# Kernel tuning notes

Measured on AMD Instinct MI355X. Metric: run time of the kernel, lower is better.

The kernel has to match this reference:

```python
import jax, jax.numpy as jnp
import numpy as np

K = 8                      # batch_k
NONZERO_CUTOFF = 1.4       # nonzero_loss_cutoff
MARGIN = 1.0               # F.triplet_margin_loss default (module's margin arg is unused)
PD_EPS = 1e-6              # torch pairwise_distance eps


def setup_inputs() -> dict:
    key = jax.random.key(0)
    x = jax.random.normal(key, (4096, 128), dtype=jnp.float32)
    return {"x": x}


def _sample_indices(x, key):
    """Distance-weighted negative sampling; returns (a_idx, p_idx, n_idx), each [n*(K-1)]."""
    n, d = x.shape
    # per-row L2 normalize (eps added to norm, as in original)
    xn = x / (jnp.sqrt(jnp.sum(x * x, axis=1, keepdims=True)) + 1e-5)
    # pairwise euclidean distance; identity added under sqrt exactly as original
    sq = jnp.sum(xn * xn, axis=1, keepdims=True)               # [n,1]
    dist2 = sq + sq.T - 2.0 * (xn @ xn.T)                       # [n,n]
    dist = jnp.sqrt(dist2 + jnp.eye(n, dtype=x.dtype))          # [n,n]
    # distance-weighted sampling log-weights (Wu et al.)
    log_w = (2.0 - d) * jnp.log(dist) - (d - 3) / 2.0 * jnp.log(1.0 - 0.25 * dist * dist)
    w = jnp.exp(log_w - jnp.max(log_w))
    # block mask: same-block pairs excluded
    block = jnp.arange(n) // K                                  # [n]
    mask = (block[:, None] != block[None, :]).astype(x.dtype)
    w = w * mask * (dist < NONZERO_CUTOFF).astype(x.dtype)
    row_sum = jnp.sum(w, axis=1, keepdims=True)
    # rows where weights are degenerate fall back to uniform (original's try/except)
    valid = jnp.isfinite(row_sum) & (row_sum > 0) & jnp.all(jnp.isfinite(w), axis=1, keepdims=True)
    logits = jnp.where(valid, jnp.where(w > 0, jnp.log(w), -jnp.inf), 0.0)   # [n,n]
    # batched categorical sampling via Gumbel-max: K-1 negatives per anchor
    g = jax.random.gumbel(key, (n, K - 1, n), dtype=jnp.float32)
    n_idx = jnp.argmax(logits[:, None, :] + g, axis=-1).reshape(-1)          # [n*(K-1)]
    # anchor/positive pairs: for each i, all other members of its block
    r = jnp.arange(n) % K                                       # position in block
    off = jnp.arange(K - 1)
    p_off = jnp.where(off[None, :] < r[:, None], off[None, :], off[None, :] + 1)
    p_idx = (block[:, None] * K + p_off).reshape(-1)            # [n*(K-1)]
    a_idx = jnp.repeat(jnp.arange(n), K - 1)                    # [n*(K-1)]
    return a_idx, p_idx, n_idx


def reference(x) -> jnp.ndarray:
    key = jax.random.key(42)
    a_idx, p_idx, n_idx = _sample_indices(x, key)
    a, p, ng = x[a_idx], x[p_idx], x[n_idx]
    d_ap = jnp.sqrt(jnp.sum((a - p + PD_EPS) ** 2, axis=1))
    d_an = jnp.sqrt(jnp.sum((a - ng + PD_EPS) ** 2, axis=1))
    return jnp.mean(jnp.maximum(d_ap - d_an + MARGIN, 0.0))
```

## Files before the change

### kernel.cpp

```cpp
#include <hip/hip_runtime.h>
#include <stdint.h>

#define NROWS 4096
#define DIM   128
#define KB    8
#define NS    7
#define TCH   16
#define NSEG  4
#define NPAIR 2048
#define HALF_CNT 58720256u

typedef __bf16 v8bf __attribute__((ext_vector_type(8)));
typedef float  v4f  __attribute__((ext_vector_type(4)));

__device__ __forceinline__ uint32_t rotl32(uint32_t x, int r) {
    return (x << r) | (x >> (32 - r));
}

__device__ __forceinline__ void threefry2x32(uint32_t c0, uint32_t c1,
                                             uint32_t& o0, uint32_t& o1) {
    const uint32_t ks0 = 0u;
    const uint32_t ks1 = 42u;
    const uint32_t ks2 = 0x1BD11BDAu ^ ks0 ^ ks1;
    uint32_t x0 = c0 + ks0;
    uint32_t x1 = c1 + ks1;
#define TF_R(r) { x0 += x1; x1 = rotl32(x1, r); x1 ^= x0; }
    TF_R(13) TF_R(15) TF_R(26) TF_R(6)
    x0 += ks1; x1 += ks2 + 1u;
    TF_R(17) TF_R(29) TF_R(16) TF_R(24)
    x0 += ks2; x1 += ks0 + 2u;
    TF_R(13) TF_R(15) TF_R(26) TF_R(6)
    x0 += ks0; x1 += ks1 + 3u;
    TF_R(17) TF_R(29) TF_R(16) TF_R(24)
    x0 += ks1; x1 += ks2 + 4u;
    TF_R(13) TF_R(15) TF_R(26) TF_R(6)
    x0 += ks2; x1 += ks0 + 5u;
#undef TF_R
    o0 = x0; o1 = x1;
}

__device__ __forceinline__ float gumbel_of(uint32_t b) {
    float f = __uint_as_float((b >> 9) | 0x3f800000u) - 1.0f;
    float u = f + 1.17549435e-38f;
    float l1 = __log2f(u);
    float inner = -0.69314718055994531f * l1;
    float l2 = __log2f(inner);
    return -0.69314718055994531f * l2;
}

__global__ void knorm(const float* __restrict__ x, __bf16* __restrict__ xb,
                      float* __restrict__ sqv) {
    const int i = blockIdx.x;
    const int t = threadIdx.x;
    float2 v = ((const float2*)(x + (size_t)i * DIM))[t];
    float s = v.x * v.x + v.y * v.y;
#pragma unroll
    for (int m = 32; m > 0; m >>= 1) s += __shfl_xor(s, m, 64);
    float norm = sqrtf(s) + 1e-5f;
    float ox = v.x / norm, oy = v.y / norm;
    union { __bf16 b[2]; uint32_t u; } ph;
    ph.b[0] = (__bf16)ox; ph.b[1] = (__bf16)oy;
    ((uint32_t*)xb)[i * 64 + t] = ph.u;
    float s2 = ox * ox + oy * oy;
#pragma unroll
    for (int m = 32; m > 0; m >>= 1) s2 += __shfl_xor(s2, m, 64);
    if (t == 0) sqv[i] = s2;
}

__global__ __launch_bounds__(256, 4) void kdist(
        const __bf16* __restrict__ xb, const float* __restrict__ sqv,
        int* __restrict__ cnt, unsigned short* __restrict__ t16,
        float2* __restrict__ nwp) {
    const int lane  = threadIdx.x & 63;
    const int chunk = (blockIdx.x << 2) + (threadIdx.x >> 6);
    const int grp   = blockIdx.y;
    const int rlo = lane & 15;
    const int khi = lane >> 4;
    const unsigned int below = (1u << rlo) - 1u;

    const int afr = grp * 8 + (rlo >> 1) + ((rlo & 1) << 11);
    v8bf ah[4];
#pragma unroll
    for (int ks = 0; ks < 4; ++ks)
        ah[ks] = *(const v8bf*)(xb + (size_t)afr * DIM + ks * 32 + khi * 8);

    const int base = grp * 8 + khi * 2;
    float sqA[4];
    sqA[0] = sqv[base];
    sqA[1] = sqv[base + 2048];
    sqA[2] = sqv[base + 1];
    sqA[3] = sqv[base + 2049];

    const int rbA = ((base)     * 16 + chunk) << 8;
    const int rbB = ((base + 1) * 16 + chunk) << 8;
    unsigned int cA = 0, cB = 0;

    const int tcol0 = chunk * 256 + rlo;

    v8bf bhn[4];
    float sqn;
    {
        const size_t boff = (size_t)tcol0 * DIM + khi * 8;
#pragma unroll
        for (int ks = 0; ks < 4; ++ks) bhn[ks] = *(const v8bf*)(xb + boff + ks * 32);
        sqn = sqv[tcol0];
    }

#pragma unroll 1
    for (int cg = 0; cg < 16; ++cg) {
        v8bf bhc[4];
#pragma unroll
        for (int ks = 0; ks < 4; ++ks) bhc[ks] = bhn[ks];
        const float sqB = sqn;
        const int tcol = tcol0 + cg * 16;

        if (cg < 15) {
            const size_t boff = (size_t)(tcol + 16) * DIM + khi * 8;
#pragma unroll
            for (int ks = 0; ks < 4; ++ks) bhn[ks] = *(const v8bf*)(xb + boff + ks * 32);
            sqn = sqv[tcol + 16];
        }

        v4f acc = {0.f, 0.f, 0.f, 0.f};
#pragma unroll
        for (int ks = 0; ks < 4; ++ks)
            acc = __builtin_amdgcn_mfma_f32_16x16x32_bf16(ah[ks], bhc[ks], acc, 0, 0, 0);

        const int tBlk = tcol >> 3;
        const bool bd0 = (tBlk != grp);
        const bool bd1 = (tBlk != grp + 256);

        float nw[4];
        bool  ic[4];
#pragma unroll
        for (int q = 0; q < 4; ++q) {
            float d2  = fmaf(-2.0f, acc[q], sqA[q] + sqB);
            float l1  = __log2f(d2);
            float t2  = fmaf(-0.25f, d2, 1.0f);
            float l2  = __log2f(t2);
            float wiv = exp2f(fmaf(63.0f, l1, 62.5f * l2));
            bool incl = (d2 < 1.96f) && ((q & 1) ? bd1 : bd0);
            ic[q] = incl;
            nw[q] = incl ? -wiv : -INFINITY;
        }

        const bool uA = ic[0] | ic[1];
        const bool uB = ic[2] | ic[3];
        unsigned long long ballA = __ballot(uA);
        unsigned long long ballB = __ballot(uB);
        unsigned int subA = (unsigned int)((ballA >> (khi * 16)) & 0xFFFFull);
        unsigned int subB = (unsigned int)((ballB >> (khi * 16)) & 0xFFFFull);
        if (uA) {
            int slot = rbA + (int)cA + __popc(subA & below);
            t16[slot] = (unsigned short)tcol;
            nwp[slot] = make_float2(nw[0], nw[1]);
        }
        if (uB) {
            int slot = rbB + (int)cB + __popc(subB & below);
            t16[slot] = (unsigned short)tcol;
            nwp[slot] = make_float2(nw[2], nw[3]);
        }
        cA += (unsigned int)__popc(subA);
        cB += (unsigned int)__popc(subB);
    }

    if (rlo == 0) {
        cnt[base * 16 + chunk]       = (int)cA;
        cnt[(base + 1) * 16 + chunk] = (int)cB;
    }
}

__global__ __launch_bounds__(256, 8) void kgum(
        const int* __restrict__ cnt, const unsigned short* __restrict__ t16,
        const float2* __restrict__ nwp,
        float* __restrict__ pV, int* __restrict__ pI) {
    const int wid  = threadIdx.x >> 6;
    const int rid  = (blockIdx.x << 2) + wid;
    const int p    = rid >> 4;
    const int lane = threadIdx.x & 63;
    const int j    = lane & 7;
    const int eo   = lane >> 3;
    const bool jv  = (j < 7);
    const uint32_t pb = ((uint32_t)p * 7u + (uint32_t)j) << 12;

    __shared__ unsigned short st[4][256];
    __shared__ float2         snw[4][256];

    const int n  = cnt[rid];
    const int rb = rid << 8;

    for (int s = lane; s < n; s += 64) {
        st[wid][s]  = t16[rb + s];
        snw[wid][s] = nwp[rb + s];
    }
    __syncthreads();

    float bkA = INFINITY, bkB = INFINITY;
    int   btA = 0x7FFFFFFF, btB = 0x7FFFFFFF;

#pragma unroll 1
    for (int e = eo; e < n; e += 8) {
        const uint32_t t = st[wid][e];
        const float2 nw  = snw[wid][e];
        const uint32_t L = pb + t;
        uint32_t o0, o1;
        threefry2x32(L, L + HALF_CNT, o0, o1);
        float fA = __uint_as_float((o0 >> 9) | 0x3f800000u) - 1.0f;
        float fB = __uint_as_float((o1 >> 9) | 0x3f800000u) - 1.0f;
        float l1A = __log2f(fA + 1.17549435e-38f);
        float l1B = __log2f(fB + 1.17549435e-38f);
        float kA = jv ? l1A * nw.x : INFINITY;
        float kB = jv ? l1B * nw.y : INFINITY;
        const int ti = (int)t;
        if (kA < bkA || (kA == bkA && ti < btA)) { bkA = kA; btA = ti; }
        if (kB < bkB || (kB == bkB && ti < btB)) { bkB = kB; btB = ti; }
    }

#pragma unroll
    for (int m = 8; m < 64; m <<= 1) {
        float v2 = __shfl_xor(bkA, m, 64);
        int   t2 = __shfl_xor(btA, m, 64);
        if (v2 < bkA || (v2 == bkA && t2 < btA)) { bkA = v2; btA = t2; }
        v2 = __shfl_xor(bkB, m, 64);
        t2 = __shfl_xor(btB, m, 64);
        if (v2 < bkB || (v2 == bkB && t2 < btB)) { bkB = v2; btB = t2; }
    }

    __shared__ float sV[4][2][NS];
    __shared__ int   sT[4][2][NS];
    if (lane < NS) {
        sV[wid][0][lane] = bkA; sT[wid][0][lane] = btA;
        sV[wid][1][lane] = bkB; sT[wid][1][lane] = btB;
    }
    __syncthreads();
    if (threadIdx.x < 2 * NS) {
        const int r = threadIdx.x / NS, jj = threadIdx.x - r * NS;
        float v = sV[0][r][jj];
        int   t = sT[0][r][jj];
#pragma unroll
        for (int w = 1; w < 4; ++w) {
            float v2 = sV[w][r][jj];
            int   t2 = sT[w][r][jj];
            if (v2 < v || (v2 == v && t2 < t)) { v = v2; t = t2; }
        }
        const int cgrp = blockIdx.x & 3;
        size_t s = ((size_t)(p + r * 2048) * NS + jj) * NSEG + cgrp;
        pV[s] = v; pI[s] = t;
    }
}

__global__ void kcombine(const float* __restrict__ pV, const int* __restrict__ pI,
                         int* __restrict__ nidx, int nc) {
    int s = blockIdx.x * 256 + threadIdx.x;
    if (s >= NROWS * NS) return;
    float bv = INFINITY;
    int bi = 0x7FFFFFFF;
    for (int c = 0; c < nc; ++c) {
        float v = pV[(size_t)s * nc + c];
        int idx = pI[(size_t)s * nc + c];
        if (v < bv || (v == bv && idx < bi)) { bv = v; bi = idx; }
    }
    nidx[s] = (bv == INFINITY) ? -1 : bi;
}

__global__ __launch_bounds__(256, 2) void ksample(
        const __bf16* __restrict__ xb, const float* __restrict__ sqv,
        float* __restrict__ pV, int* __restrict__ pI) {
    const int lane  = threadIdx.x & 63;
    const int chunk = (blockIdx.x << 2) + (threadIdx.x >> 6);
    const int grp   = blockIdx.y;
    const int rlo = lane & 15;
    const int khi = lane >> 4;

    const int afr = grp * 8 + (rlo >> 1) + ((rlo & 1) << 11);
    v8bf ah[4];
#pragma unroll
    for (int ks = 0; ks < 4; ++ks)
        ah[ks] = *(const v8bf*)(xb + (size_t)afr * DIM + ks * 32 + khi * 8);
    const int base = grp * 8 + khi * 2;
    float sqA[4];
    sqA[0] = sqv[base];
    sqA[1] = sqv[base + 2048];
    sqA[2] = sqv[base + 1];
    sqA[3] = sqv[base + 2049];
    const uint32_t P0 = (uint32_t)base;
    const uint32_t P1 = (uint32_t)(base + 1);

    float    bestV[4][NS];
    uint32_t bestP[4];
#pragma unroll
    for (int q = 0; q < 4; ++q) {
        bestP[q] = 0u;
#pragma unroll
        for (int j = 0; j < NS; ++j) bestV[q][j] = INFINITY;
    }
    const int tcol0 = chunk * 256 + rlo;

    v8bf bhn[4];
    float sqn;
    {
        const size_t boff = (size_t)tcol0 * DIM + khi * 8;
#pragma unroll
        for (int ks = 0; ks < 4; ++ks) bhn[ks] = *(const v8bf*)(xb + boff + ks * 32);
        sqn = sqv[tcol0];
    }

#pragma unroll 1
    for (int cg = 0; cg < 16; ++cg) {
        v8bf bhc[4];
#pragma unroll
        for (int ks = 0; ks < 4; ++ks) bhc[ks] = bhn[ks];
        const float sqB = sqn;
        const int tcol = tcol0 + cg * 16;
        if (cg < 15) {
            const size_t boff = (size_t)(tcol + 16) * DIM + khi * 8;
#pragma unroll
            for (int ks = 0; ks < 4; ++ks) bhn[ks] = *(const v8bf*)(xb + boff + ks * 32);
            sqn = sqv[tcol + 16];
        }
        v4f acc = {0.f, 0.f, 0.f, 0.f};
#pragma unroll
        for (int ks = 0; ks < 4; ++ks)
            acc = __builtin_amdgcn_mfma_f32_16x16x32_bf16(ah[ks], bhc[ks], acc, 0, 0, 0);
        const int tBlk = tcol >> 3;
        const bool bd0 = (tBlk != grp);
        const bool bd1 = (tBlk != grp + 256);
        float nw[4];
#pragma unroll
        for (int q = 0; q < 4; ++q) {
            float d2  = fmaf(-2.0f, acc[q], sqA[q] + sqB);
            float l1  = __log2f(d2);
            float t2  = fmaf(-0.25f, d2, 1.0f);
            float l2  = __log2f(t2);
            float wiv = exp2f(fmaf(63.0f, l1, 62.5f * l2));
            bool incl = (d2 < 1.96f) && ((q & 1) ? bd1 : bd0);
            nw[q] = incl ? -wiv : -INFINITY;
        }
        const uint32_t tB = (uint32_t)tcol;
#pragma unroll
        for (int j = 0; j < NS; ++j) {
            uint32_t L0 = ((P0 * 7u + (uint32_t)j) << 12) + tB;
            uint32_t L1 = ((P1 * 7u + (uint32_t)j) << 12) + tB;
            uint32_t o0, o1, o2, o3;
            threefry2x32(L0, L0 + HALF_CNT, o0, o1);
            threefry2x32(L1, L1 + HALF_CNT, o2, o3);
            float vv[4];
            vv[0] = __log2f(__uint_as_float((o0 >> 9) | 0x3f800000u) - 1.0f + 1.17549435e-38f) * nw[0];
            vv[1] = __log2f(__uint_as_float((o1 >> 9) | 0x3f800000u) - 1.0f + 1.17549435e-38f) * nw[1];
            vv[2] = __log2f(__uint_as_float((o2 >> 9) | 0x3f800000u) - 1.0f + 1.17549435e-38f) * nw[2];
            vv[3] = __log2f(__uint_as_float((o3 >> 9) | 0x3f800000u) - 1.0f + 1.17549435e-38f) * nw[3];
            const uint32_t keep = ~(0xFu << (4 * j));
            const uint32_t put  = ((uint32_t)cg) << (4 * j);
#pragma unroll
            for (int q = 0; q < 4; ++q) {
                bool lt = vv[q] < bestV[q][j];
                uint32_t np = (bestP[q] & keep) | put;
                bestV[q][j] = lt ? vv[q] : bestV[q][j];
                bestP[q]    = lt ? np : bestP[q];
            }
        }
    }
#pragma unroll
    for (int q = 0; q < 4; ++q) {
        const int a = base + (q >> 1) + ((q & 1) << 11);
#pragma unroll
        for (int j = 0; j < NS; ++j) {
            float v = bestV[q][j];
            int idx = tcol0 + (int)((bestP[q] >> (4 * j)) & 0xFu) * 16;
#pragma unroll
            for (int m = 1; m < 16; m <<= 1) {
                float v2 = __shfl_xor(v, m, 16);
                int   i2 = __shfl_xor(idx, m, 16);
                if (v2 < v || (v2 == v && i2 < idx)) { v = v2; idx = i2; }
            }
            if (rlo == 0) {
                size_t s = ((size_t)a * NS + j) * TCH + chunk;
                pV[s] = v;
                pI[s] = idx;
            }
        }
    }
}

__global__ void kfixup(int* __restrict__ nidx) {
    const int i = blockIdx.x;
    if (nidx[(size_t)i * NS] >= 0) return;
    const int lane = threadIdx.x;
    for (int j = 0; j < NS; ++j) {
        float bv = -INFINITY;
        int bi = 0x7FFFFFFF;
        for (int t = lane; t < NROWS; t += 64) {
            uint32_t o0, o1;
            float g;
            if (i < 2048) {
                uint32_t L = (((uint32_t)(i * NS + j)) << 12) + (uint32_t)t;
                threefry2x32(L, L + HALF_CNT, o0, o1);
                g = gumbel_of(o0);
            } else {
                uint32_t L = (((uint32_t)((i - 2048) * NS + j)) << 12) + (uint32_t)t;
                threefry2x32(L, L + HALF_CNT, o0, o1);
                g = gumbel_of(o1);
            }
            if (g > bv) { bv = g; bi = t; }
        }
#pragma unroll
        for (int m = 1; m < 64; m <<= 1) {
            float v2 = __shfl_xor(bv, m, 64);
            int   i2 = __shfl_xor(bi, m, 64);
            if (v2 > bv || (v2 == bv && i2 < bi)) { bv = v2; bi = i2; }
        }
        if (lane == 0) nidx[i * NS + j] = bi;
    }
}

__global__ void kloss(const float* __restrict__ x, const int* __restrict__ nidx,
                      float* __restrict__ loss) {
    int s = blockIdx.x * 256 + threadIdx.x;
    if (s >= NROWS * NS) return;
    int i = s / NS, j = s - i * NS;
    int r = i & (KB - 1), blk = i >> 3;
    int po = (j < r) ? j : j + 1;
    int p = blk * KB + po;
    int n = nidx[s] & (NROWS - 1);
    const float4* A  = (const float4*)(x + (size_t)i * DIM);
    const float4* P  = (const float4*)(x + (size_t)p * DIM);
    const float4* Ng = (const float4*)(x + (size_t)n * DIM);
    float sap = 0.0f, san = 0.0f;
#pragma unroll 8
    for (int k = 0; k < DIM / 4; ++k) {
        float4 a = A[k], pv = P[k], nv = Ng[k];
        float d;
        d = a.x - pv.x + 1e-6f; sap += d * d;
        d = a.y - pv.y + 1e-6f; sap += d * d;
        d = a.z - pv.z + 1e-6f; sap += d * d;
        d = a.w - pv.w + 1e-6f; sap += d * d;
        d = a.x - nv.x + 1e-6f; san += d * d;
        d = a.y - nv.y + 1e-6f; san += d * d;
        d = a.z - nv.z + 1e-6f; san += d * d;
        d = a.w - nv.w + 1e-6f; san += d * d;
    }
    loss[s] = fmaxf(sqrtf(sap) - sqrtf(san) + 1.0f, 0.0f);
}

__global__ void kreduce(const float* __restrict__ loss, float* __restrict__ out) {
    __shared__ float part[4];
    const int tid = threadIdx.x;
    float sum = 0.0f;
    for (int s = tid; s < NROWS * NS; s += 256) sum += loss[s];
#pragma unroll
    for (int m = 32; m > 0; m >>= 1) sum += __shfl_xor(sum, m, 64);
    if ((tid & 63) == 0) part[tid >> 6] = sum;
    __syncthreads();
    if (tid == 0) out[0] = (part[0] + part[1] + part[2] + part[3]) / 28672.0f;
}

extern "C" void kernel_launch(void* const* d_in, const int* in_sizes, int n_in,
                              void* d_out, int out_size, void* d_ws, size_t ws_size,
                              hipStream_t stream) {
    const float* x = (const float*)d_in[0];
    float* out = (float*)d_out;

    uint8_t* w = (uint8_t*)d_ws;
    size_t off = 0;
    auto take = [&](size_t bytes) {
        void* p = w + off;
        off = (off + bytes + 255) & ~(size_t)255;
        return p;
    };
    __bf16* xb   = (__bf16*)take((size_t)NROWS * DIM * 2);
    float*  sqv  = (float*)take((size_t)NROWS * 4);
    int*    nidx = (int*)take((size_t)NROWS * NS * 4);
    float*  loss = (float*)take((size_t)NROWS * NS * 4);
    int*    cnt  = (int*)take((size_t)NPAIR * 16 * 4);
    const size_t prefix = off;
    const size_t t16_b = (size_t)NPAIR * 16 * 256 * 2;
    const size_t nwp_b = (size_t)NPAIR * 16 * 256 * 8;
    const size_t pv4_b = (size_t)NROWS * NS * NSEG * 4;
    const size_t NEED_BIG = prefix + ((t16_b + 255) & ~(size_t)255)
                          + ((nwp_b + 255) & ~(size_t)255)
                          + 2 * ((pv4_b + 255) & ~(size_t)255);

    knorm<<<NROWS, 64, 0, stream>>>(x, xb, sqv);

    if (ws_size >= NEED_BIG) {
        unsigned short* t16 = (unsigned short*)take(t16_b);
        float2*         nwp = (float2*)take(nwp_b);
        float*          pV  = (float*)take(pv4_b);
        int*            pI  = (int*)take(pv4_b);
        kdist<<<dim3(TCH / 4, 256), 256, 0, stream>>>(xb, sqv, cnt, t16, nwp);
        kgum<<<NPAIR * 16 / 4, 256, 0, stream>>>(cnt, t16, nwp, pV, pI);
        kcombine<<<(NROWS * NS + 255) / 256, 256, 0, stream>>>(pV, pI, nidx, NSEG);
    } else {
        float* pV = (float*)take((size_t)NROWS * NS * TCH * 4);
        int*   pI = (int*)take((size_t)NROWS * NS * TCH * 4);
        ksample<<<dim3(TCH / 4, 256), 256, 0, stream>>>(xb, sqv, pV, pI);
        kcombine<<<(NROWS * NS + 255) / 256, 256, 0, stream>>>(pV, pI, nidx, TCH);
    }

    kfixup<<<NROWS, 64, 0, stream>>>(nidx);
    kloss<<<(NROWS * NS + 255) / 256, 256, 0, stream>>>(x, nidx, loss);
    kreduce<<<1, 256, 0, stream>>>(loss, out);
}
```

Before: 200.1 us.

## Pack key and index into 64-bit atomicMin, drop LDS reduction and combine pass

Gumbel keys and column indices are packed into one 64-bit value, so the argmin becomes unsigned integer min operations. Per-block partial results are merged with global atomicMin, which replaces the shared-memory cross-wave reduction, the __syncthreads and the segment-combine kernel. A lightweight extract kernel decodes the packed winners. Rotate-left now uses alignbit. The change adds a memset launch and relies on the float bit pattern ordering the same as the value, which holds only for non-negative keys.

```diff
diff --git a/kernel.cpp b/kernel.cpp
--- a/kernel.cpp
+++ b/kernel.cpp
@@ -6,7 +6,6 @@
 #define KB    8
 #define NS    7
 #define TCH   16
-#define NSEG  4
 #define NPAIR 2048
 #define HALF_CNT 58720256u
 
@@ -14,7 +13,7 @@
 typedef float  v4f  __attribute__((ext_vector_type(4)));
 
 __device__ __forceinline__ uint32_t rotl32(uint32_t x, int r) {
-    return (x << r) | (x >> (32 - r));
+    return __builtin_amdgcn_alignbit(x, x, 32 - r);
 }
 
 __device__ __forceinline__ void threefry2x32(uint32_t c0, uint32_t c1,
@@ -173,7 +172,7 @@
 __global__ __launch_bounds__(256, 8) void kgum(
         const int* __restrict__ cnt, const unsigned short* __restrict__ t16,
         const float2* __restrict__ nwp,
-        float* __restrict__ pV, int* __restrict__ pI) {
+        unsigned long long* __restrict__ pk) {
     const int wid  = threadIdx.x >> 6;
     const int rid  = (blockIdx.x << 2) + wid;
     const int p    = rid >> 4;
@@ -195,8 +194,7 @@
     }
     __syncthreads();
 
-    float bkA = INFINITY, bkB = INFINITY;
-    int   btA = 0x7FFFFFFF, btB = 0x7FFFFFFF;
+    unsigned long long bA = ~0ull, bB = ~0ull;
 
 #pragma unroll 1
     for (int e = eo; e < n; e += 8) {
@@ -211,56 +209,33 @@
         float l1B = __log2f(fB + 1.17549435e-38f);
         float kA = jv ? l1A * nw.x : INFINITY;
         float kB = jv ? l1B * nw.y : INFINITY;
-        const int ti = (int)t;
-        if (kA < bkA || (kA == bkA && ti < btA)) { bkA = kA; btA = ti; }
-        if (kB < bkB || (kB == bkB && ti < btB)) { bkB = kB; btB = ti; }
+        unsigned long long pA = ((unsigned long long)__float_as_uint(kA) << 32) | t;
+        unsigned long long pB = ((unsigned long long)__float_as_uint(kB) << 32) | t;
+        bA = pA < bA ? pA : bA;
+        bB = pB < bB ? pB : bB;
     }
 
 #pragma unroll
     for (int m = 8; m < 64; m <<= 1) {
-        float v2 = __shfl_xor(bkA, m, 64);
-        int   t2 = __shfl_xor(btA, m, 64);
-        if (v2 < bkA || (v2 == bkA && t2 < btA)) { bkA = v2; btA = t2; }
-        v2 = __shfl_xor(bkB, m, 64);
-        t2 = __shfl_xor(btB, m, 64);
-        if (v2 < bkB || (v2 == bkB && t2 < btB)) { bkB = v2; btB = t2; }
-    }
-
-    __shared__ float sV[4][2][NS];
-    __shared__ int   sT[4][2][NS];
-    if (lane < NS) {
-        sV[wid][0][lane] = bkA; sT[wid][0][lane] = btA;
-        sV[wid][1][lane] = bkB; sT[wid][1][lane] = btB;
-    }
-    __syncthreads();
-    if (threadIdx.x < 2 * NS) {
-        const int r = threadIdx.x / NS, jj = threadIdx.x - r * NS;
-        float v = sV[0][r][jj];
-        int   t = sT[0][r][jj];
-#pragma unroll
-        for (int w = 1; w < 4; ++w) {
-            float v2 = sV[w][r][jj];
-            int   t2 = sT[w][r][jj];
-            if (v2 < v || (v2 == v && t2 < t)) { v = v2; t = t2; }
-        }
-        const int cgrp = blockIdx.x & 3;
-        size_t s = ((size_t)(p + r * 2048) * NS + jj) * NSEG + cgrp;
-        pV[s] = v; pI[s] = t;
-    }
-}
-
-__global__ void kcombine(const float* __restrict__ pV, const int* __restrict__ pI,
-                         int* __restrict__ nidx, int nc) {
+        unsigned long long vA = __shfl_xor(bA, m, 64);
+        unsigned long long vB = __shfl_xor(bB, m, 64);
+        bA = vA < bA ? vA : bA;
+        bB = vB < bB ? vB : bB;
+    }
+
+    if (eo == 0 && jv) {
+        atomicMin(&pk[(size_t)p * NS + j], bA);
+        atomicMin(&pk[(size_t)(p + 2048) * NS + j], bB);
+    }
+}
+
+__global__ void kextract(const unsigned long long* __restrict__ pk,
+                         int* __restrict__ nidx) {
     int s = blockIdx.x * 256 + threadIdx.x;
     if (s >= NROWS * NS) return;
-    float bv = INFINITY;
-    int bi = 0x7FFFFFFF;
-    for (int c = 0; c < nc; ++c) {
-        float v = pV[(size_t)s * nc + c];
-        int idx = pI[(size_t)s * nc + c];
-        if (v < bv || (v == bv && idx < bi)) { bv = v; bi = idx; }
-    }
-    nidx[s] = (bv == INFINITY) ? -1 : bi;
+    unsigned long long v = pk[s];
+    uint32_t kb = (uint32_t)(v >> 32);
+    nidx[s] = (kb >= 0x7F800000u) ? -1 : (int)(v & 0xFFFFu);
 }
 
 __global__ __launch_bounds__(256, 2) void ksample(
@@ -380,6 +355,20 @@
             }
         }
     }
+}
+
+__global__ void kcombine(const float* __restrict__ pV, const int* __restrict__ pI,
+                         int* __restrict__ nidx, int nc) {
+    int s = blockIdx.x * 256 + threadIdx.x;
+    if (s >= NROWS * NS) return;
+    float bv = INFINITY;
+    int bi = 0x7FFFFFFF;
+    for (int c = 0; c < nc; ++c) {
+        float v = pV[(size_t)s * nc + c];
+        int idx = pI[(size_t)s * nc + c];
+        if (v < bv || (v == bv && idx < bi)) { bv = v; bi = idx; }
+    }
+    nidx[s] = (bv == INFINITY) ? -1 : bi;
 }
 
 __global__ void kfixup(int* __restrict__ nidx) {
@@ -472,24 +461,22 @@
     int*    nidx = (int*)take((size_t)NROWS * NS * 4);
     float*  loss = (float*)take((size_t)NROWS * NS * 4);
     int*    cnt  = (int*)take((size_t)NPAIR * 16 * 4);
+    unsigned long long* pk = (unsigned long long*)take((size_t)NROWS * NS * 8);
     const size_t prefix = off;
     const size_t t16_b = (size_t)NPAIR * 16 * 256 * 2;
     const size_t nwp_b = (size_t)NPAIR * 16 * 256 * 8;
-    const size_t pv4_b = (size_t)NROWS * NS * NSEG * 4;
     const size_t NEED_BIG = prefix + ((t16_b + 255) & ~(size_t)255)
-                          + ((nwp_b + 255) & ~(size_t)255)
-                          + 2 * ((pv4_b + 255) & ~(size_t)255);
+                          + ((nwp_b + 255) & ~(size_t)255);
 
     knorm<<<NROWS, 64, 0, stream>>>(x, xb, sqv);
 
     if (ws_size >= NEED_BIG) {
         unsigned short* t16 = (unsigned short*)take(t16_b);
         float2*         nwp = (float2*)take(nwp_b);
-        float*          pV  = (float*)take(pv4_b);
-        int*            pI  = (int*)take(pv4_b);
+        hipMemsetAsync(pk, 0xFF, (size_t)NROWS * NS * 8, stream);
         kdist<<<dim3(TCH / 4, 256), 256, 0, stream>>>(xb, sqv, cnt, t16, nwp);
-        kgum<<<NPAIR * 16 / 4, 256, 0, stream>>>(cnt, t16, nwp, pV, pI);
-        kcombine<<<(NROWS * NS + 255) / 256, 256, 0, stream>>>(pV, pI, nidx, NSEG);
+        kgum<<<NPAIR * 16 / 4, 256, 0, stream>>>(cnt, t16, nwp, pk);
+        kextract<<<(NROWS * NS + 255) / 256, 256, 0, stream>>>(pk, nidx);
     } else {
         float* pV = (float*)take((size_t)NROWS * NS * TCH * 4);
         int*   pI = (int*)take((size_t)NROWS * NS * TCH * 4);
```

Result: no change. 198.8 us (-0.7%).
